# Optimization experiments

Measured on AMD Instinct MI355X. Metric: run time of the kernel, lower is better.

The kernel has to match this reference:

```python
import jax, jax.numpy as jnp
import numpy as np

THRESHOLD = 0.3

def setup_inputs() -> dict:
    key = jax.random.key(0)
    ks = jax.random.split(key, 8)
    B, T, N, d = 4, 32, 1024, 2
    hd, od, hs, osz = 64, 64, 128, 2
    p = lambda k, sh: jax.random.normal(k, sh, jnp.float32) * 0.1
    return {
        "points": jax.random.uniform(ks[0], (B, T, N, d), jnp.float32),
        "W1": p(ks[1], (hd, d)),   "b1": jnp.zeros((hd,), jnp.float32),
        "W2": p(ks[2], (od, hd)),  "b2": jnp.zeros((od,), jnp.float32),
        "Wg": p(ks[3], (hd, od)),  "bg": jnp.zeros((hd,), jnp.float32),
        "Wih": p(ks[4], (3 * hs, hd)), "Whh": p(ks[5], (3 * hs, hs)),
        "bih": jnp.zeros((3 * hs,), jnp.float32), "bhh": jnp.zeros((3 * hs,), jnp.float32),
        "Wf": p(ks[6], (osz, hs)), "bf": jnp.zeros((osz,), jnp.float32),
    }

def _gcn_step(pts, W1, b1, W2, b2, Wg, bg):
    # pts: [N, d]. Torch detaches node features & adjacency (no grad to points).
    pts = jax.lax.stop_gradient(pts)
    dist = jnp.linalg.norm(pts[:, None, :] - pts[None, :, :], axis=2)  # [N,N]
    A = (dist < THRESHOLD).astype(pts.dtype)
    dinv = 1.0 / jnp.sqrt(A.sum(axis=1))          # rowsum >= 1 (self-loop)
    An = A * dinv[:, None] * dinv[None, :]        # D^{-1/2} A D^{-1/2}
    x = jax.nn.relu((An @ pts) @ W1.T + b1)       # [N, hd]
    x = jax.nn.relu((An @ x) @ W2.T + b2)         # [N, od]
    return x.mean(axis=0) @ Wg.T + bg             # [hd]

def reference(points, W1, b1, W2, b2, Wg, bg, Wih, Whh, bih, bhh, Wf, bf):
    # GCN per (batch, time): [B, T, hd]
    gcn = jax.vmap(jax.vmap(lambda p: _gcn_step(p, W1, b1, W2, b2, Wg, bg)))(points)
    H = Whh.shape[1]

    def gru_step(h, x):  # torch GRU gate order: r, z, n
        gi = x @ Wih.T + bih
        gh = h @ Whh.T + bhh
        ir, iz, inn = jnp.split(gi, 3)
        hr, hz, hn = jnp.split(gh, 3)
        r = jax.nn.sigmoid(ir + hr)
        z = jax.nn.sigmoid(iz + hz)
        n = jnp.tanh(inn + r * hn)
        h_new = (1.0 - z) * n + z * h
        return h_new, h_new

    h0 = jnp.zeros((H,), points.dtype)
    run = lambda xs: jax.lax.scan(gru_step, h0, xs)[1]   # [T, H]
    hs = jax.vmap(run)(gcn)                              # [B, T, H]
    y = hs @ Wf.T + bf                                   # [B, T, out]
    # torch: per-element gru_out.mean(dim=1, keepdim=True) on [1,T,out] -> [1,1,out], stacked -> [B,1,1,out]
    return y.mean(axis=1, keepdims=True)[:, :, None, :]
```

## Files before the change

kernel.cpp:

```cpp
#include <hip/hip_runtime.h>
#include <hip/hip_bf16.h>
#include <math.h>

#define N_PTS 1024
#define BT    128
typedef unsigned int u32;
typedef __attribute__((ext_vector_type(8))) short short8_t;
typedef __attribute__((ext_vector_type(4))) float f32x4;

__device__ __forceinline__ float bfi(u32 bits16) {
    union { u32 u; float f; } v; v.u = bits16 << 16; return v.f;
}
__device__ __forceinline__ unsigned short f2bf(float f) {
    union { float f; u32 u; } v; v.f = f;
    return (unsigned short)((v.u + 0x7FFFu + ((v.u >> 16) & 1u)) >> 16);
}
__device__ __forceinline__ float ldf(const void* p, int i, bool bf) {
    return bf ? bfi(((const unsigned short*)p)[i]) : ((const float*)p)[i];
}
__device__ __forceinline__ float2 ldp(const void* pbase, int j, bool bf) {
    if (bf) {
        u32 w = ((const u32*)pbase)[j];
        return make_float2(bfi(w & 0xFFFFu), bfi(w >> 16));
    }
    return ((const float2*)pbase)[j];
}
__device__ __forceinline__ bool detect_bf16(const void* pts, int tid, int* s_flag) {
    if (tid < 64) {
        u32 w = ((const u32*)pts)[tid];
        float v = bfi(w & 0xFFFFu);
        bool ok = (v >= 0.0f) && (v <= 1.0f);
        unsigned long long m = __ballot(ok);
        if (tid == 0) *s_flag = (m == 0xFFFFFFFFFFFFFFFFull) ? 1 : 0;
    }
    __syncthreads();
    return *s_flag != 0;
}
__device__ __forceinline__ bool is_nb(float px, float py, float qx, float qy) {
    float dx = px - qx, dy = py - qy;
    float d2 = __fadd_rn(__fmul_rn(dx, dx), __fmul_rn(dy, dy));
    return d2 < 0.09f;
}
__device__ __forceinline__ const void* pts_base(const void* pts, int bt, bool bf) {
    return bf ? (const void*)((const unsigned short*)pts + (size_t)bt * N_PTS * 2)
              : (const void*)((const float*)pts + (size_t)bt * N_PTS * 2);
}
__device__ __forceinline__ void gload16(const u32* g, u32* l) {
    __builtin_amdgcn_global_load_lds((const __attribute__((address_space(1))) u32*)g,
                                     (__attribute__((address_space(3))) u32*)l, 16, 0, 0);
}
__device__ __forceinline__ float rdlane(float v, int i) {
    return __int_as_float(__builtin_amdgcn_readlane(__float_as_int(v), i));
}
__device__ __forceinline__ float sigm_f(float x) {
    return __fdividef(1.0f, 1.0f + __expf(-x));
}
__device__ __forceinline__ float tanh_f(float x) {
    float e = __expf(2.0f * x);
    return 1.0f - __fdividef(2.0f, e + 1.0f);
}

__global__ __launch_bounds__(256) void k1_bm(const void* __restrict__ pts,
                                             float* __restrict__ dinv,
                                             float* __restrict__ gsum,
                                             u32* __restrict__ bm) {
    int blk = blockIdx.x, tid = threadIdx.x;
    int bt = blk >> 2, q = blk & 3;
    __shared__ float2 sp[N_PTS];
    __shared__ int s_flag;
    bool bf = detect_bf16(pts, tid, &s_flag);
    const void* pb = pts_base(pts, bt, bf);
    for (int j = tid; j < N_PTS; j += 256) sp[j] = ldp(pb, j, bf);
    if (blk < 32) gsum[blk * 256 + tid] = 0.0f;
    __syncthreads();
    int i = q * 256 + tid;
    float px = sp[i].x, py = sp[i].y;
    const float4* sp4 = (const float4*)sp;
    u32* bmrow = bm + (size_t)bt * 32768 + i;
    int cnt = 0;
    for (int c = 0; c < 32; c++) {
        u32 m = 0;
#pragma unroll
        for (int h = 0; h < 8; h++) {
            float4 s01 = sp4[c * 16 + 2 * h], s23 = sp4[c * 16 + 2 * h + 1];
            if (is_nb(px, py, s01.x, s01.y)) m |= 1u << (4 * h);
            if (is_nb(px, py, s01.z, s01.w)) m |= 1u << (4 * h + 1);
            if (is_nb(px, py, s23.x, s23.y)) m |= 1u << (4 * h + 2);
            if (is_nb(px, py, s23.z, s23.w)) m |= 1u << (4 * h + 3);
        }
        bmrow[c * 1024] = m;
        cnt += __popc(m);
    }
    dinv[bt * N_PTS + i] = 1.0f / sqrtf((float)cnt);
}

__global__ __launch_bounds__(256) void k2_x1v(const void* __restrict__ pts,
                                              const void* __restrict__ W1,
                                              const void* __restrict__ b1,
                                              const float* __restrict__ dinv,
                                              const u32* __restrict__ bm,
                                              u32* __restrict__ x1vB) {
    int blk = blockIdx.x, tid = threadIdx.x;
    int bt = blk >> 2, q = blk & 3;
    __shared__ float2 sud[N_PTS];
    __shared__ float2 sax[256];
    __shared__ float  sdl[256];
    __shared__ int s_flag;
    bool bf = detect_bf16(pts, tid, &s_flag);
    const void* pb = pts_base(pts, bt, bf);
    for (int j = tid; j < N_PTS; j += 256) {
        float2 p = ldp(pb, j, bf);
        float d = dinv[bt * N_PTS + j];
        sud[j] = make_float2(d * p.x, d * p.y);
    }
    __syncthreads();
    int i = q * 256 + tid;
    float ax = 0.f, ay = 0.f;
    const u32* bmr = bm + (size_t)bt * 32768 + i;
    for (int c = 0; c < 32; c++) {
        u32 m = bmr[c * 1024];
        const float4* uv = (const float4*)sud + c * 16;
#pragma unroll
        for (int h = 0; h < 16; h++) {
            float4 v = uv[h];
            bool b0 = (m >> (2 * h)) & 1u, b1_ = (m >> (2 * h + 1)) & 1u;
            ax += b0 ? v.x : 0.0f;  ay += b0 ? v.y : 0.0f;
            ax += b1_ ? v.z : 0.0f; ay += b1_ ? v.w : 0.0f;
        }
    }
    float di = dinv[bt * N_PTS + i];
    sax[tid] = make_float2(ax * di, ay * di);
    sdl[tid] = di;
    __syncthreads();
    int ch = tid & 63, wq = tid >> 6;
    float w0 = ldf(W1, 2 * ch, bf), w1v = ldf(W1, 2 * ch + 1, bf), bb = ldf(b1, ch, bf);
    for (int tt = 0; tt < 4; tt++) {
        u32 ow[8];
#pragma unroll
        for (int k2i = 0; k2i < 8; k2i++) {
            int lj = tt * 64 + wq * 16 + 2 * k2i;
            float2 a0 = sax[lj], a1 = sax[lj + 1];
            float v0 = sdl[lj]     * fmaxf(fmaf(w0, a0.x, fmaf(w1v, a0.y, bb)), 0.0f);
            float v1 = sdl[lj + 1] * fmaxf(fmaf(w0, a1.x, fmaf(w1v, a1.y, bb)), 0.0f);
            ow[k2i] = (u32)f2bf(v0) | ((u32)f2bf(v1) << 16);
        }
        u32* dst = x1vB + ((size_t)(bt * 16 + q * 4 + tt) * 64 + ch) * 36 + wq * 8;
        *(uint4*)dst = make_uint4(ow[0], ow[1], ow[2], ow[3]);
        *(uint4*)(dst + 4) = make_uint4(ow[4], ow[5], ow[6], ow[7]);
    }
}

__global__ __launch_bounds__(256) void k3_mfma(const void* __restrict__ pts,
                                               const void* __restrict__ W2,
                                               const void* __restrict__ b2,
                                               const float* __restrict__ dinv,
                                               const u32* __restrict__ bm,
                                               const u32* __restrict__ x1vB,
                                               float* __restrict__ gsum) {
    __shared__ u32 pool[15424];
    __shared__ int s_flag;
    float* poolf = (float*)pool;
    int tid = threadIdx.x, lane = tid & 63, w = tid >> 6;
    int l15 = lane & 15, quad = lane >> 4;
    int blk = blockIdx.x, bt = blk & 127, rowblk = blk >> 7;
    bool bf = detect_bf16(pts, tid, &s_flag);

    const u32* xg = x1vB + (size_t)bt * 36864;
    for (int it = w; it < 9; it += 4)
        gload16(xg + it * 256 + lane * 4, pool + 8192 + it * 256 + lane * 4);

    const u32* bg_ = bm + (size_t)bt * 32768 + rowblk * 256;
    for (int idx = tid; idx < 8192; idx += 256) {
        int c = idx >> 8, r = idx & 255;
        pool[idx] = bg_[c * 1024 + r];
    }
    unsigned short* W2B = (unsigned short*)(pool + 12800);
    for (int idx = tid; idx < 4096; idx += 256) {
        int o = idx >> 6, c = idx & 63;
        W2B[o * 72 + c] = f2bf(ldf(W2, idx, bf));
    }
    if (tid < 256) poolf[15104 + tid] = dinv[bt * N_PTS + rowblk * 256 + tid];
    if (tid < 64)  poolf[15360 + tid] = ldf(b2, tid, bf);

    f32x4 acc[4][4];
#pragma unroll
    for (int rf = 0; rf < 4; rf++)
#pragma unroll
        for (int nb = 0; nb < 4; nb++)
#pragma unroll
            for (int r = 0; r < 4; r++) acc[rf][nb][r] = 0.0f;

    for (int t = 0; t < 16; t++) {
        __syncthreads();
        if (t + 1 < 16) {
            u32* dst = pool + ((t & 1) ? 8192 : 10496);
            const u32* src = xg + (t + 1) * 2304;
            for (int it = w; it < 9; it += 4)
                gload16(src + it * 256 + lane * 4, dst + it * 256 + lane * 4);
        }
        const unsigned short* xf = (const unsigned short*)(pool + ((t & 1) ? 10496 : 8192));
#pragma unroll
        for (int ks = 0; ks < 2; ks++) {
            short8_t bq[4];
#pragma unroll
            for (int rf = 0; rf < 4; rf++) {
                u32 mw = pool[(2 * t + ks) * 256 + w * 64 + rf * 16 + l15];
                u32 by = (mw >> (quad * 8)) & 0xFFu;
                short8_t v;
#pragma unroll
                for (int i2 = 0; i2 < 8; i2++)
                    v[i2] = (by & (1u << i2)) ? (short)0x3F80 : (short)0;
                bq[rf] = v;
            }
#pragma unroll
            for (int nb = 0; nb < 4; nb++) {
                short8_t af = *(const short8_t*)(xf + (nb * 16 + l15) * 72 + ks * 32 + quad * 8);
#pragma unroll
                for (int rf = 0; rf < 4; rf++)
                    acc[rf][nb] = __builtin_amdgcn_mfma_f32_16x16x32_bf16(af, bq[rf], acc[rf][nb], 0, 0, 0);
            }
        }
    }
    __syncthreads();

    u32* dump = pool;
#pragma unroll
    for (int rf = 0; rf < 4; rf++) {
        int rn = w * 64 + rf * 16 + l15;
        float di = poolf[15104 + rn];
#pragma unroll
        for (int nb = 0; nb < 4; nb++) {
            u32 lo = (u32)f2bf(acc[rf][nb][0] * di) | ((u32)f2bf(acc[rf][nb][1] * di) << 16);
            u32 hi = (u32)f2bf(acc[rf][nb][2] * di) | ((u32)f2bf(acc[rf][nb][3] * di) << 16);
            u32* dst = dump + rn * 36 + nb * 8 + quad * 2;
            dst[0] = lo; dst[1] = hi;
        }
    }
    __syncthreads();
    f32x4 xacc[4][4];
#pragma unroll
    for (int ob = 0; ob < 4; ob++)
#pragma unroll
        for (int rf = 0; rf < 4; rf++)
#pragma unroll
            for (int r = 0; r < 4; r++) xacc[ob][rf][r] = 0.0f;
#pragma unroll
    for (int ks2 = 0; ks2 < 2; ks2++) {
        short8_t b2f[4];
#pragma unroll
        for (int rf = 0; rf < 4; rf++)
            b2f[rf] = *(const short8_t*)((const unsigned short*)dump +
                        (w * 64 + rf * 16 + l15) * 72 + ks2 * 32 + quad * 8);
#pragma unroll
        for (int ob = 0; ob < 4; ob++) {
            short8_t a2 = *(const short8_t*)(W2B + (ob * 16 + l15) * 72 + ks2 * 32 + quad * 8);
#pragma unroll
            for (int rf = 0; rf < 4; rf++)
                xacc[ob][rf] = __builtin_amdgcn_mfma_f32_16x16x32_bf16(a2, b2f[rf], xacc[ob][rf], 0, 0, 0);
        }
    }
#pragma unroll
    for (int ob = 0; ob < 4; ob++) {
#pragma unroll
        for (int r = 0; r < 4; r++) {
            int o = ob * 16 + quad * 4 + r;
            float bb = poolf[15360 + o];
            float s = 0.0f;
#pragma unroll
            for (int rf = 0; rf < 4; rf++) s += fmaxf(xacc[ob][rf][r] + bb, 0.0f);
            s += __shfl_down(s, 8, 16);
            s += __shfl_down(s, 4, 16);
            s += __shfl_down(s, 2, 16);
            s += __shfl_down(s, 1, 16);
            if (l15 == 0) atomicAdd(&gsum[bt * 64 + o], s);
        }
    }
}

__global__ __launch_bounds__(384, 1) void k4a_gi(const void* __restrict__ pts,
                                                 const void* __restrict__ Wg,
                                                 const void* __restrict__ bg,
                                                 const void* __restrict__ Wih,
                                                 const void* __restrict__ bih,
                                                 const float* __restrict__ gsum,
                                                 float* __restrict__ gi_ws) {
    int blk = blockIdx.x, tid = threadIdx.x;
    __shared__ float s_gm[64];
    __shared__ float s_x[64];
    __shared__ int s_flag;
    bool bf = detect_bf16(pts, tid, &s_flag);
    if (tid < 64) s_gm[tid] = gsum[(size_t)blk * 64 + tid] * (1.0f / 1024.0f);
    int r = tid;
    float wv[64];
    if (bf) {
#pragma unroll
        for (int k = 0; k < 64; k++) wv[k] = bfi(((const unsigned short*)Wih)[r * 64 + k]);
    } else {
        const float4* wr = (const float4*)Wih + r * 16;
#pragma unroll
        for (int qq = 0; qq < 16; qq++) {
            float4 v = wr[qq];
            wv[4*qq] = v.x; wv[4*qq+1] = v.y; wv[4*qq+2] = v.z; wv[4*qq+3] = v.w;
        }
    }
    float br = ldf(bih, r, bf);
    float wg[64];
    if (tid < 64) {
        if (bf) {
#pragma unroll
            for (int k = 0; k < 64; k++) wg[k] = bfi(((const unsigned short*)Wg)[tid * 64 + k]);
        } else {
            const float4* wr = (const float4*)Wg + tid * 16;
#pragma unroll
            for (int qq = 0; qq < 16; qq++) {
                float4 v = wr[qq];
                wg[4*qq] = v.x; wg[4*qq+1] = v.y; wg[4*qq+2] = v.z; wg[4*qq+3] = v.w;
            }
        }
    }
    __syncthreads();
    if (tid < 64) {
        float gmv = s_gm[tid];
        float s0 = ldf(bg, tid, bf), s1 = 0.f, s2 = 0.f, s3 = 0.f;
#pragma unroll
        for (int k = 0; k < 64; k += 4) {
            s0 = fmaf(wg[k],     rdlane(gmv, k),     s0);
            s1 = fmaf(wg[k + 1], rdlane(gmv, k + 1), s1);
            s2 = fmaf(wg[k + 2], rdlane(gmv, k + 2), s2);
            s3 = fmaf(wg[k + 3], rdlane(gmv, k + 3), s3);
        }
        s_x[tid] = (s0 + s1) + (s2 + s3);
    }
    __syncthreads();
    float xv = s_x[tid & 63];
    float s0 = br, s1 = 0.f, s2 = 0.f, s3 = 0.f;
#pragma unroll
    for (int k = 0; k < 64; k += 4) {
        s0 = fmaf(wv[k],     rdlane(xv, k),     s0);
        s1 = fmaf(wv[k + 1], rdlane(xv, k + 1), s1);
        s2 = fmaf(wv[k + 2], rdlane(xv, k + 2), s2);
        s3 = fmaf(wv[k + 3], rdlane(xv, k + 3), s3);
    }
    gi_ws[(size_t)blk * 384 + r] = (s0 + s1) + (s2 + s3);
}

__global__ __launch_bounds__(768, 1) void k4b_scan(const void* __restrict__ pts,
                                                   const void* __restrict__ Whh,
                                                   const void* __restrict__ bhh,
                                                   const void* __restrict__ Wf,
                                                   const void* __restrict__ bf_,
                                                   const float* __restrict__ gi_ws,
                                                   float* __restrict__ out) {
    int b = blockIdx.x, tid = threadIdx.x;
    __shared__ float s_gi[12288];
    __shared__ float s_part[2][768];
    __shared__ float s_hm[128];
    __shared__ int s_flag;
    bool bf = detect_bf16(pts, tid, &s_flag);
    const u32* gi_g = (const u32*)gi_ws + (size_t)b * 12288;
    u32* s_gi_u = (u32*)s_gi;
#pragma unroll
    for (int j = 0; j < 4; j++)
        gload16(gi_g + j * 3072 + tid * 4, s_gi_u + j * 3072 + tid * 4);

    int hi = (tid >= 384) ? 1 : 0;
    int r = tid - hi * 384;
    int lane = tid & 63;
    float wh2[64];
    {
        int koff = hi * 64;
        if (bf) {
#pragma unroll
            for (int k = 0; k < 64; k++)
                wh2[k] = bfi(((const unsigned short*)Whh)[r * 128 + koff + k]);
        } else {
            const float4* wr = (const float4*)Whh + (r * 128 + koff) / 4;
#pragma unroll
            for (int qq = 0; qq < 16; qq++) {
                float4 v = wr[qq];
                wh2[4*qq] = v.x; wh2[4*qq+1] = v.y; wh2[4*qq+2] = v.z; wh2[4*qq+3] = v.w;
            }
        }
    }
    float bhr = hi ? 0.0f : ldf(bhh, r, bf);
    int c = hi * 64 + lane;
    float hval = 0.0f;
    float hsum = 0.0f;
    __syncthreads();

    for (int t = 0; t < 32; t++) {
        float gi_r = s_gi[t * 384 + c];
        float gi_z = s_gi[t * 384 + 128 + c];
        float gi_n = s_gi[t * 384 + 256 + c];
        float s0 = bhr, s1 = 0.f, s2 = 0.f, s3 = 0.f;
#pragma unroll
        for (int k = 0; k < 64; k += 4) {
            s0 = fmaf(wh2[k],     rdlane(hval, k),     s0);
            s1 = fmaf(wh2[k + 1], rdlane(hval, k + 1), s1);
            s2 = fmaf(wh2[k + 2], rdlane(hval, k + 2), s2);
            s3 = fmaf(wh2[k + 3], rdlane(hval, k + 3), s3);
        }
        s_part[t & 1][tid] = (s0 + s1) + (s2 + s3);
        __syncthreads();
        const float* P = s_part[t & 1];
        float gr = gi_r + P[c]       + P[384 + c];
        float gz = gi_z + P[128 + c] + P[512 + c];
        float hn =        P[256 + c] + P[640 + c];
        float rr = sigm_f(gr);
        float z  = sigm_f(gz);
        float n  = tanh_f(fmaf(rr, hn, gi_n));
        hval = fmaf(z, hval - n, n);
        hsum += hval;
    }
    if (tid < 64) s_hm[tid] = hsum * (1.0f / 32.0f);
    else if (tid >= 384 && tid < 448) s_hm[64 + lane] = hsum * (1.0f / 32.0f);
    __syncthreads();
    if (tid < 128) {
        float hm = s_hm[tid];
        s_part[0][tid]       = ldf(Wf, tid, bf) * hm;
        s_part[0][128 + tid] = ldf(Wf, 128 + tid, bf) * hm;
    }
    __syncthreads();
    if (tid < 2) {
        float s = ldf(bf_, tid, bf);
        for (int k = 0; k < 128; k++) s += s_part[0][tid * 128 + k];
        out[b * 2 + tid] = s;
    }
}

extern "C" void kernel_launch(void* const* d_in, const int* in_sizes, int n_in,
                              void* d_out, int out_size, void* d_ws, size_t ws_size,
                              hipStream_t stream) {
    const void* pts = d_in[0];
    const void* W1  = d_in[1];
    const void* b1  = d_in[2];
    const void* W2  = d_in[3];
    const void* b2  = d_in[4];
    const void* Wg  = d_in[5];
    const void* bg  = d_in[6];
    const void* Wih = d_in[7];
    const void* Whh = d_in[8];
    const void* bih = d_in[9];
    const void* bhh = d_in[10];
    const void* Wf  = d_in[11];
    const void* bf_ = d_in[12];

    float* dinv = (float*)d_ws;
    float* gsum = dinv + (size_t)BT * N_PTS;
    u32*   bm   = (u32*)(gsum + BT * 64);
    u32*   x1vB = bm + (size_t)BT * 32768;
    float* gi_ws = (float*)x1vB;

    k1_bm  <<<512, 256, 0, stream>>>(pts, dinv, gsum, bm);
    k2_x1v <<<512, 256, 0, stream>>>(pts, W1, b1, dinv, bm, x1vB);
    k3_mfma<<<512, 256, 0, stream>>>(pts, W2, b2, dinv, bm, x1vB, gsum);
    k4a_gi <<<128, 384, 0, stream>>>(pts, Wg, bg, Wih, bih, gsum, gi_ws);
    k4b_scan<<<4, 768, 0, stream>>>(pts, Whh, bhh, Wf, bf_, gi_ws, (float*)d_out);
}
```

Baseline: 233.6 us.

## Compute first adjacency aggregation with bf16 MFMA using split-precision point features

The first aggregation (A times dinv-scaled points) in k2_x1v is rewritten from per-thread scalar bitmask loops into MFMA 16x16x32 bf16 matrix multiplies. Adjacency bits are expanded into bf16 ones, and the point features are stored as bf16 hi/lo pairs so the sum approximates fp32 precision. The block's slice of the bitmask is also staged into LDS first. The intent is to offload the masked accumulation onto the matrix cores. In exchange it adds LDS usage, bit-expansion ALU work and a shuffle-based reduction of the hi/lo columns.

```diff
diff --git a/kernel.cpp b/kernel.cpp
--- a/kernel.cpp
+++ b/kernel.cpp
@@ -102,7 +102,8 @@
                                               u32* __restrict__ x1vB) {
     int blk = blockIdx.x, tid = threadIdx.x;
     int bt = blk >> 2, q = blk & 3;
-    __shared__ float2 sud[N_PTS];
+    __shared__ u32 sbm[8192];
+    __shared__ unsigned short u_lds[4][1032];
     __shared__ float2 sax[256];
     __shared__ float  sdl[256];
     __shared__ int s_flag;
@@ -111,26 +112,54 @@
     for (int j = tid; j < N_PTS; j += 256) {
         float2 p = ldp(pb, j, bf);
         float d = dinv[bt * N_PTS + j];
-        sud[j] = make_float2(d * p.x, d * p.y);
-    }
-    __syncthreads();
-    int i = q * 256 + tid;
-    float ax = 0.f, ay = 0.f;
-    const u32* bmr = bm + (size_t)bt * 32768 + i;
+        float ux = d * p.x, uy = d * p.y;
+        unsigned short hx = f2bf(ux), hy = f2bf(uy);
+        u_lds[0][j] = hx;
+        u_lds[1][j] = hy;
+        u_lds[2][j] = f2bf(ux - bfi(hx));
+        u_lds[3][j] = f2bf(uy - bfi(hy));
+    }
+    const u32* bg_ = bm + (size_t)bt * 32768 + q * 256;
+    for (int idx = tid; idx < 8192; idx += 256) {
+        int c = idx >> 8, r = idx & 255;
+        sbm[idx] = bg_[c * 1024 + r];
+    }
+    sdl[tid] = dinv[bt * N_PTS + q * 256 + tid];
+    __syncthreads();
+
+    int lane = tid & 63, w = tid >> 6;
+    int l15 = lane & 15, quad = lane >> 4;
+    f32x4 acc[4];
+#pragma unroll
+    for (int rf = 0; rf < 4; rf++)
+#pragma unroll
+        for (int r = 0; r < 4; r++) acc[rf][r] = 0.0f;
+
+    const unsigned short* urow = &u_lds[l15 & 3][0];
     for (int c = 0; c < 32; c++) {
-        u32 m = bmr[c * 1024];
-        const float4* uv = (const float4*)sud + c * 16;
-#pragma unroll
-        for (int h = 0; h < 16; h++) {
-            float4 v = uv[h];
-            bool b0 = (m >> (2 * h)) & 1u, b1_ = (m >> (2 * h + 1)) & 1u;
-            ax += b0 ? v.x : 0.0f;  ay += b0 ? v.y : 0.0f;
-            ax += b1_ ? v.z : 0.0f; ay += b1_ ? v.w : 0.0f;
-        }
-    }
-    float di = dinv[bt * N_PTS + i];
-    sax[tid] = make_float2(ax * di, ay * di);
-    sdl[tid] = di;
+        short8_t bu = *(const short8_t*)(urow + c * 32 + quad * 8);
+#pragma unroll
+        for (int rf = 0; rf < 4; rf++) {
+            u32 mw = sbm[c * 256 + w * 64 + rf * 16 + l15];
+            u32 by = (mw >> (quad * 8)) & 0xFFu;
+            short8_t v;
+#pragma unroll
+            for (int i2 = 0; i2 < 8; i2++)
+                v[i2] = (by & (1u << i2)) ? (short)0x3F80 : (short)0;
+            acc[rf] = __builtin_amdgcn_mfma_f32_16x16x32_bf16(v, bu, acc[rf], 0, 0, 0);
+        }
+    }
+#pragma unroll
+    for (int rf = 0; rf < 4; rf++) {
+#pragma unroll
+        for (int r = 0; r < 4; r++) {
+            float vsum = acc[rf][r] + __shfl_xor(acc[rf][r], 2, 64);
+            int row = w * 64 + rf * 16 + quad * 4 + r;
+            float sc = vsum * sdl[row];
+            if (l15 == 0)      sax[row].x = sc;
+            else if (l15 == 1) sax[row].y = sc;
+        }
+    }
     __syncthreads();
     int ch = tid & 63, wq = tid >> 6;
     float w0 = ldf(W1, 2 * ch, bf), w1v = ldf(W1, 2 * ch + 1, bf), bb = ldf(b1, ch, bf);
```

New measurement: 224.5 us. 3.9% less time.
